# Kernel optimization log

Measured on AMD Instinct MI355X. Metric: run time of the kernel, lower is better.

## Reference

```python
import jax, jax.numpy as jnp
import numpy as np

B, L, D = 4, 256, 2048
LE, DE = 2048, 1024
H = 16
HD = D // H  # 128
ROPE_BASE = 10000.0


def apply_rope(q):
    # q: [B, H, L, HD]; rotate interleaved pairs along seq axis L (torchtune-style)
    half = HD // 2
    inv_freq = 1.0 / (ROPE_BASE ** (jnp.arange(0, HD, 2, dtype=jnp.float32) / HD))  # [half]
    pos = jnp.arange(L, dtype=jnp.float32)
    ang = pos[:, None] * inv_freq[None, :]           # [L, half]
    cos = jnp.cos(ang)[None, None, :, :]             # [1,1,L,half]
    sin = jnp.sin(ang)[None, None, :, :]
    qr = q.reshape(B, H, L, half, 2)
    q1, q2 = qr[..., 0], qr[..., 1]
    out = jnp.stack([q1 * cos - q2 * sin, q1 * sin + q2 * cos], axis=-1)
    return out.reshape(B, H, L, HD)


def setup_inputs() -> dict:
    key = jax.random.key(0)
    ks = jax.random.split(key, 7)
    s_d = 1.0 / np.sqrt(D)
    s_e = 1.0 / np.sqrt(DE)
    return {
        "x": jax.random.normal(ks[0], (B, L, D), jnp.float32),
        "encoder_inputs": jax.random.normal(ks[1], (B, LE, DE), jnp.float32),
        "Wq": jax.random.normal(ks[2], (D, D), jnp.float32) * s_d,
        "bq": jnp.zeros((D,), jnp.float32),
        "Wk": jax.random.normal(ks[3], (DE, D), jnp.float32) * s_e,
        "bk": jnp.zeros((D,), jnp.float32),
        "Wv": jax.random.normal(ks[4], (DE, D), jnp.float32) * s_e,
        "bv": jnp.zeros((D,), jnp.float32),
        "Wo": jax.random.normal(ks[5], (D, D), jnp.float32) * s_d,
        "bo": jnp.zeros((D,), jnp.float32),
    }


def reference(x, encoder_inputs, Wq, bq, Wk, bk, Wv, bv, Wo, bo):
    q = (x @ Wq + bq).reshape(B, L, H, HD).transpose(0, 2, 1, 3)              # [B,H,L,HD]
    k = (encoder_inputs @ Wk + bk).reshape(B, LE, H, HD).transpose(0, 2, 1, 3)  # [B,H,Le,HD]
    v = (encoder_inputs @ Wv + bv).reshape(B, LE, H, HD).transpose(0, 2, 1, 3)
    q = apply_rope(q)
    scale = 1.0 / jnp.sqrt(jnp.float32(HD))
    scores = jnp.einsum("bhld,bhmd->bhlm", q, k) * scale                      # [B,H,L,Le]
    attn = jax.nn.softmax(scores, axis=-1)
    ctx = jnp.einsum("bhlm,bhmd->bhld", attn, v)                              # [B,H,L,HD]
    ctx = ctx.transpose(0, 2, 1, 3).reshape(B, L, D)
    return ctx @ Wo + bo
```

## Files before the change

kernel.cpp:

```cpp
#include <hip/hip_runtime.h>


#define B_ 4
#define L_ 256
#define D_ 2048
#define LE_ 2048
#define DE_ 1024
#define H_ 16
#define HD_ 128

using f32x4  = __attribute__((ext_vector_type(4))) float;
using bf16x8 = __attribute__((ext_vector_type(8))) short;

__device__ __forceinline__ unsigned short f2bf(float f) {
    union { float f; unsigned int u; } v; v.f = f;
    unsigned int r = v.u + 0x7fffu + ((v.u >> 16) & 1u);
    return (unsigned short)(r >> 16);
}
__device__ __forceinline__ float b2f(unsigned short h) {
    union { unsigned int u; float f; } v; v.u = ((unsigned int)h) << 16;
    return v.f;
}

__device__ __forceinline__ void load_lds16(const void* g, void* l) {
    __builtin_amdgcn_global_load_lds((const __attribute__((address_space(1))) void*)g,
                                     (__attribute__((address_space(3))) void*)l, 16, 0, 0);
}

__global__ void cast_f32_bf16(const float* __restrict__ in, unsigned short* __restrict__ out, int n) {
    int i = (blockIdx.x * 256 + threadIdx.x) * 4;
    if (i < n) {
        float4 v = *(const float4*)(in + i);
        ushort4 o;
        o.x = f2bf(v.x); o.y = f2bf(v.y); o.z = f2bf(v.z); o.w = f2bf(v.w);
        *(ushort4*)(out + i) = o;
    }
}

__global__ void transpose_f32_bf16(const float* __restrict__ in, unsigned short* __restrict__ out,
                                   int R, int C) {
    __shared__ float t[32][33];
    int r0 = blockIdx.y * 32, c0 = blockIdx.x * 32;
    int tx = threadIdx.x, ty = threadIdx.y;
    #pragma unroll
    for (int i = 0; i < 32; i += 8) t[ty + i][tx] = in[(long)(r0 + ty + i) * C + c0 + tx];
    __syncthreads();
    #pragma unroll
    for (int i = 0; i < 32; i += 8) out[(long)(c0 + ty + i) * R + r0 + tx] = f2bf(t[tx][ty + i]);
}

__global__ void transpose_bf16_batched(const unsigned short* __restrict__ in,
                                       unsigned short* __restrict__ out, int R, int C) {
    __shared__ unsigned short t[32][33];
    long zo = (long)blockIdx.z * R * C;
    int r0 = blockIdx.y * 32, c0 = blockIdx.x * 32;
    int tx = threadIdx.x, ty = threadIdx.y;
    #pragma unroll
    for (int i = 0; i < 32; i += 8) t[ty + i][tx] = in[zo + (long)(r0 + ty + i) * C + c0 + tx];
    __syncthreads();
    #pragma unroll
    for (int i = 0; i < 32; i += 8) out[zo + (long)(c0 + ty + i) * R + r0 + tx] = t[tx][ty + i];
}

__global__ void combine_q_rope(const float* __restrict__ P, const float* __restrict__ bq,
                               unsigned short* __restrict__ Q) {
    int gid = blockIdx.x * 256 + threadIdx.x;
    int p = gid & 63;
    int h = (gid >> 6) & 15;
    int m = gid >> 10;
    int n = h * 128 + 2 * p;
    long i0 = (long)m * 2048 + n;
    float2 a  = *(const float2*)(P + i0);
    float2 b2 = *(const float2*)(P + 2097152 + i0);
    float q1 = a.x + b2.x + bq[n];
    float q2 = a.y + b2.y + bq[n + 1];
    int l = m & 255, b = m >> 8;
    float inv = powf(10000.0f, -(float)p * (1.0f / 64.0f));
    float s, c;
    sincosf((float)l * inv, &s, &c);
    const float sc = 0.08838834764831845f;
    long qi = (((long)(b * 16 + h) * 256 + l) << 7) + 2 * p;
    ushort2 o;
    o.x = f2bf((q1 * c - q2 * s) * sc);
    o.y = f2bf((q1 * s + q2 * c) * sc);
    *(ushort2*)(Q + qi) = o;
}

__global__ void combine_pv(const float* __restrict__ P, unsigned short* __restrict__ ctx) {
    int gid = blockIdx.x * 256 + threadIdx.x;
    long e = (long)gid * 4;
    float4 a = *(const float4*)(P + e);
    float4 b = *(const float4*)(P + 2097152 + e);
    int bh = (int)(e >> 15);
    int m  = (int)((e >> 7) & 255);
    int d  = (int)(e & 127);
    int bb = bh >> 4, h = bh & 15;
    ushort4 o;
    o.x = f2bf(a.x + b.x); o.y = f2bf(a.y + b.y);
    o.z = f2bf(a.z + b.z); o.w = f2bf(a.w + b.w);
    *(ushort4*)(ctx + ((long)(bb * 256 + m)) * 2048 + h * 128 + d) = o;
}

__global__ void combine_o(const float* __restrict__ P, const float* __restrict__ bo,
                          float* __restrict__ out) {
    int gid = blockIdx.x * 256 + threadIdx.x;
    long e = (long)gid * 4;
    float4 a = *(const float4*)(P + e);
    float4 b = *(const float4*)(P + 2097152 + e);
    int n = (int)(e & 2047);
    float4 bb = *(const float4*)(bo + n);
    float4 r;
    r.x = a.x + b.x + bb.x; r.y = a.y + b.y + bb.y;
    r.z = a.z + b.z + bb.z; r.w = a.w + b.w + bb.w;
    *(float4*)(out + e) = r;
}

__launch_bounds__(256)
__global__ void softmax_rows(unsigned short* __restrict__ S) {
    long row = blockIdx.x;
    unsigned short* p = S + row * 2048;
    int t = threadIdx.x, w = t >> 6, lane = t & 63;
    bf16x8 raw = *(const bf16x8*)(p + t * 8);
    float v[8];
    float mx = -1e30f;
    #pragma unroll
    for (int i = 0; i < 8; i++) { v[i] = b2f((unsigned short)raw[i]); mx = fmaxf(mx, v[i]); }
    #pragma unroll
    for (int o = 32; o; o >>= 1) mx = fmaxf(mx, __shfl_xor(mx, o));
    __shared__ float redm[4], reds[4];
    if (lane == 0) redm[w] = mx;
    __syncthreads();
    mx = fmaxf(fmaxf(redm[0], redm[1]), fmaxf(redm[2], redm[3]));
    float sum = 0.f;
    #pragma unroll
    for (int i = 0; i < 8; i++) { v[i] = __expf(v[i] - mx); sum += v[i]; }
    #pragma unroll
    for (int o = 32; o; o >>= 1) sum += __shfl_xor(sum, o);
    if (lane == 0) reds[w] = sum;
    __syncthreads();
    sum = reds[0] + reds[1] + reds[2] + reds[3];
    float r = 1.0f / sum;
    bf16x8 res;
    #pragma unroll
    for (int i = 0; i < 8; i++) res[i] = (short)f2bf(v[i] * r);
    *(bf16x8*)(p + t * 8) = res;
}

template <int EPI>
__launch_bounds__(256)
__global__ void gemm_bt(const unsigned short* __restrict__ A, const unsigned short* __restrict__ Bt,
                        const float* __restrict__ biasA, const float* __restrict__ biasB,
                        void* __restrict__ outA, void* __restrict__ outB,
                        int M, int N, int K, int lda, int ldb,
                        long strideA, long strideB, int zdiv, int nsplit) {
    __shared__ __align__(16) unsigned short smem[16384];
    const int z = blockIdx.z;
    int s = 0, bh = z;
    if constexpr (EPI == 4) { s = z / zdiv; bh = z - s * zdiv; }
    const unsigned short* Ab = A + (long)bh * strideA + (long)s * K;
    const unsigned short* Bb = Bt + (long)bh * strideB + (long)s * K;
    const int m0 = blockIdx.y * 128, n0 = blockIdx.x * 128;
    const int tid = threadIdx.x;
    const int w = tid >> 6, lane = tid & 63;
    const int quad = lane >> 4, l16 = lane & 15;
    const int wr = w >> 1, wc = w & 1;
    const int srow = lane >> 2;
    const int scol = (lane & 3) * 8;

    f32x4 acc[4][4] = {};

    auto stage = [&](int k0, int p) {
        unsigned short* As = smem + p * 8192;
        unsigned short* Bs = As + 4096;
        #pragma unroll
        for (int q = 0; q < 2; q++) {
            int ci = q * 4 + w;
            int row = ci * 16 + srow;
            load_lds16(Ab + (long)(m0 + row) * lda + k0 + scol, (void*)(As + ci * 512));
            load_lds16(Bb + (long)(n0 + row) * ldb + k0 + scol, (void*)(Bs + ci * 512));
        }
    };

    const int nk = K >> 5;
    stage(0, 0);
    for (int i = 0; i < nk; i++) {
        __syncthreads();
        if (i + 1 < nk) stage((i + 1) << 5, (i + 1) & 1);
        const unsigned short* As = smem + (i & 1) * 8192;
        const unsigned short* Bs = As + 4096;
        bf16x8 af[4], bfr[4];
        #pragma unroll
        for (int ii = 0; ii < 4; ii++) {
            int r = wr * 64 + ii * 16 + l16;
            af[ii] = *(const bf16x8*)(As + r * 32 + quad * 8);
        }
        #pragma unroll
        for (int j = 0; j < 4; j++) {
            int r = wc * 64 + j * 16 + l16;
            bfr[j] = *(const bf16x8*)(Bs + r * 32 + quad * 8);
        }
        #pragma unroll
        for (int ii = 0; ii < 4; ii++)
            #pragma unroll
            for (int j = 0; j < 4; j++)
                acc[ii][j] = __builtin_amdgcn_mfma_f32_16x16x32_bf16(af[ii], bfr[j], acc[ii][j], 0, 0, 0);
    }
    __syncthreads();

    if constexpr (EPI == 1 || EPI == 2) {
        const bool second = (EPI == 1) && (n0 >= nsplit);
        const float* bias = second ? biasB : biasA;
        const int n0e = second ? n0 - nsplit : n0;
        unsigned short* dst = (unsigned short*)(second ? outB : outA);
        #pragma unroll
        for (int p = 0; p < 2; p++) {
            if (wr == p) {
                #pragma unroll
                for (int i = 0; i < 4; i++)
                    #pragma unroll
                    for (int j = 0; j < 4; j++)
                        #pragma unroll
                        for (int r = 0; r < 4; r++) {
                            int ml = i * 16 + quad * 4 + r;
                            int n  = wc * 64 + j * 16 + l16;
                            float v = acc[i][j][r];
                            if (bias) v += bias[n0e + n];
                            smem[ml * 136 + n] = f2bf(v);
                        }
            }
            __syncthreads();
            #pragma unroll
            for (int pass = 0; pass < 4; pass++) {
                int row = pass * 16 + (tid >> 4);
                int seg = tid & 15;
                bf16x8 val = *(const bf16x8*)(smem + row * 136 + seg * 8);
                int m = m0 + p * 64 + row;
                if constexpr (EPI == 1) {
                    int h = n0e >> 7;
                    int b = m >> 11, mrow = m & 2047;
                    long idx = (((long)(b * 16 + h)) << 11) + mrow;
                    *(bf16x8*)(dst + (idx << 7) + seg * 8) = val;
                } else {
                    *(bf16x8*)((unsigned short*)outA + (long)z * M * N + (long)m * N + n0 + seg * 8) = val;
                }
            }
            __syncthreads();
        }
    } else {
        float* smf = (float*)smem;
        long zo = ((long)s * zdiv + bh) * (long)M * N;
        #pragma unroll
        for (int q4 = 0; q4 < 4; q4++) {
            if (wr == (q4 >> 1)) {
                #pragma unroll
                for (int ii = 0; ii < 2; ii++) {
                    int i = (q4 & 1) * 2 + ii;
                    #pragma unroll
                    for (int j = 0; j < 4; j++)
                        #pragma unroll
                        for (int r = 0; r < 4; r++) {
                            int ml = ii * 16 + quad * 4 + r;
                            int n  = wc * 64 + j * 16 + l16;
                            smf[ml * 132 + n] = acc[i][j][r];
                        }
                }
            }
            __syncthreads();
            #pragma unroll
            for (int pass = 0; pass < 4; pass++) {
                int row = pass * 8 + (tid >> 5);
                int seg = tid & 31;
                float4 val = *(const float4*)(smf + row * 132 + seg * 4);
                int m = m0 + q4 * 32 + row;
                *(float4*)((float*)outA + zo + (long)m * N + n0 + seg * 4) = val;
            }
            __syncthreads();
        }
    }
}

extern "C" void kernel_launch(void* const* d_in, const int* in_sizes, int n_in,
                              void* d_out, int out_size, void* d_ws, size_t ws_size,
                              hipStream_t stream) {
    const float* x   = (const float*)d_in[0];
    const float* enc = (const float*)d_in[1];
    const float* Wq  = (const float*)d_in[2];
    const float* bq  = (const float*)d_in[3];
    const float* Wk  = (const float*)d_in[4];
    const float* bk  = (const float*)d_in[5];
    const float* Wv  = (const float*)d_in[6];
    const float* bv  = (const float*)d_in[7];
    const float* Wo  = (const float*)d_in[8];
    const float* bo  = (const float*)d_in[9];
    float* out = (float*)d_out;

    char* ws = (char*)d_ws;
    const size_t MB = 1024 * 1024;
    unsigned short* x_bf   = (unsigned short*)(ws + 0 * MB);
    unsigned short* enc_bf = (unsigned short*)(ws + 4 * MB);
    unsigned short* WqT    = (unsigned short*)(ws + 20 * MB);
    unsigned short* WkvT   = (unsigned short*)(ws + 28 * MB);
    unsigned short* V_bf   = (unsigned short*)(ws + 36 * MB);
    unsigned short* K_bf   = (unsigned short*)(ws + 68 * MB);
    unsigned short* WoT    = (unsigned short*)(ws + 100 * MB);
    unsigned short* Q_bf   = (unsigned short*)(ws + 108 * MB);
    unsigned short* Vt     = (unsigned short*)(ws + 112 * MB);
    unsigned short* S_bf   = (unsigned short*)(ws + 0 * MB);
    float*          Pq     = (float*)(ws + 36 * MB);
    float*          Ppv    = (float*)(ws + 68 * MB);
    float*          Po     = (float*)(ws + 0 * MB);
    unsigned short* ctx_bf = (unsigned short*)(ws + 108 * MB);

    dim3 tb(32, 8);

    cast_f32_bf16<<<2048, 256, 0, stream>>>(x, x_bf, 2097152);
    cast_f32_bf16<<<8192, 256, 0, stream>>>(enc, enc_bf, 8388608);

    transpose_f32_bf16<<<dim3(64, 64), tb, 0, stream>>>(Wq, WqT, 2048, 2048);
    transpose_f32_bf16<<<dim3(64, 32), tb, 0, stream>>>(Wk, WkvT, 1024, 2048);
    transpose_f32_bf16<<<dim3(64, 32), tb, 0, stream>>>(Wv, WkvT + 2048 * 1024, 1024, 2048);
    transpose_f32_bf16<<<dim3(64, 64), tb, 0, stream>>>(Wo, WoT, 2048, 2048);

    gemm_bt<4><<<dim3(16, 8, 2), 256, 0, stream>>>(x_bf, WqT, nullptr, nullptr, Pq, nullptr,
                                                   1024, 2048, 1024, 2048, 2048, 0, 0, 1, 0);
    combine_q_rope<<<4096, 256, 0, stream>>>(Pq, bq, Q_bf);

    gemm_bt<1><<<dim3(32, 64, 1), 256, 0, stream>>>(enc_bf, WkvT, bk, bv, K_bf, V_bf,
                                                    8192, 4096, 1024, 1024, 1024, 0, 0, 1, 2048);

    transpose_bf16_batched<<<dim3(4, 64, 64), tb, 0, stream>>>(V_bf, Vt, 2048, 128);

    gemm_bt<2><<<dim3(16, 2, 64), 256, 0, stream>>>(Q_bf, K_bf, nullptr, nullptr, S_bf, nullptr,
                                                    256, 2048, 128, 128, 128,
                                                    256 * 128, 2048 * 128, 1, 0);
    softmax_rows<<<16384, 256, 0, stream>>>(S_bf);

    gemm_bt<4><<<dim3(1, 2, 128), 256, 0, stream>>>(S_bf, Vt, nullptr, nullptr, Ppv, nullptr,
                                                    256, 128, 1024, 2048, 2048,
                                                    256 * 2048, 128 * 2048, 64, 0);
    combine_pv<<<2048, 256, 0, stream>>>(Ppv, ctx_bf);

    gemm_bt<4><<<dim3(16, 8, 2), 256, 0, stream>>>(ctx_bf, WoT, nullptr, nullptr, Po, nullptr,
                                                   1024, 2048, 1024, 2048, 2048, 0, 0, 1, 0);
    combine_o<<<2048, 256, 0, stream>>>(Po, bo, out);
}
```

Before: 404.2 us.

## Load GEMM fragments directly from global into registers, dropping LDS staging

The GEMM main loop no longer stages A/B tiles through LDS with global_load_lds. Each wave now loads its MFMA fragments straight from global memory into registers, using a two-deep register double buffer, and the per-iteration barriers are removed. LDS usage drops, which may raise occupancy. In exchange there is no data sharing across waves, so each A/B row is fetched by two waves and global and L2 traffic increases.

```diff
diff --git a/kernel.cpp b/kernel.cpp
--- a/kernel.cpp
+++ b/kernel.cpp
@@ -20,11 +20,6 @@
 __device__ __forceinline__ float b2f(unsigned short h) {
     union { unsigned int u; float f; } v; v.u = ((unsigned int)h) << 16;
     return v.f;
-}
-
-__device__ __forceinline__ void load_lds16(const void* g, void* l) {
-    __builtin_amdgcn_global_load_lds((const __attribute__((address_space(1))) void*)g,
-                                     (__attribute__((address_space(3))) void*)l, 16, 0, 0);
 }
 
 __global__ void cast_f32_bf16(const float* __restrict__ in, unsigned short* __restrict__ out, int n) {
@@ -153,7 +148,7 @@
                         void* __restrict__ outA, void* __restrict__ outB,
                         int M, int N, int K, int lda, int ldb,
                         long strideA, long strideB, int zdiv, int nsplit) {
-    __shared__ __align__(16) unsigned short smem[16384];
+    __shared__ __align__(16) unsigned short smem[8704];
     const int z = blockIdx.z;
     int s = 0, bh = z;
     if constexpr (EPI == 4) { s = z / zdiv; bh = z - s * zdiv; }
@@ -164,48 +159,46 @@
     const int w = tid >> 6, lane = tid & 63;
     const int quad = lane >> 4, l16 = lane & 15;
     const int wr = w >> 1, wc = w & 1;
-    const int srow = lane >> 2;
-    const int scol = (lane & 3) * 8;
+
+    const unsigned short* Arow[4];
+    const unsigned short* Brow[4];
+    #pragma unroll
+    for (int i = 0; i < 4; i++)
+        Arow[i] = Ab + (long)(m0 + wr * 64 + i * 16 + l16) * lda + quad * 8;
+    #pragma unroll
+    for (int j = 0; j < 4; j++)
+        Brow[j] = Bb + (long)(n0 + wc * 64 + j * 16 + l16) * ldb + quad * 8;
 
     f32x4 acc[4][4] = {};
-
-    auto stage = [&](int k0, int p) {
-        unsigned short* As = smem + p * 8192;
-        unsigned short* Bs = As + 4096;
-        #pragma unroll
-        for (int q = 0; q < 2; q++) {
-            int ci = q * 4 + w;
-            int row = ci * 16 + srow;
-            load_lds16(Ab + (long)(m0 + row) * lda + k0 + scol, (void*)(As + ci * 512));
-            load_lds16(Bb + (long)(n0 + row) * ldb + k0 + scol, (void*)(Bs + ci * 512));
+    bf16x8 a0[4], b0[4], a1[4], b1[4];
+
+    #pragma unroll
+    for (int i = 0; i < 4; i++) a0[i] = *(const bf16x8*)(Arow[i]);
+    #pragma unroll
+    for (int j = 0; j < 4; j++) b0[j] = *(const bf16x8*)(Brow[j]);
+
+    for (int k = 0; k + 64 <= K; k += 64) {
+        #pragma unroll
+        for (int i = 0; i < 4; i++) a1[i] = *(const bf16x8*)(Arow[i] + k + 32);
+        #pragma unroll
+        for (int j = 0; j < 4; j++) b1[j] = *(const bf16x8*)(Brow[j] + k + 32);
+        #pragma unroll
+        for (int i = 0; i < 4; i++)
+            #pragma unroll
+            for (int j = 0; j < 4; j++)
+                acc[i][j] = __builtin_amdgcn_mfma_f32_16x16x32_bf16(a0[i], b0[j], acc[i][j], 0, 0, 0);
+        if (k + 64 < K) {
+            #pragma unroll
+            for (int i = 0; i < 4; i++) a0[i] = *(const bf16x8*)(Arow[i] + k + 64);
+            #pragma unroll
+            for (int j = 0; j < 4; j++) b0[j] = *(const bf16x8*)(Brow[j] + k + 64);
         }
-    };
-
-    const int nk = K >> 5;
-    stage(0, 0);
-    for (int i = 0; i < nk; i++) {
-        __syncthreads();
-        if (i + 1 < nk) stage((i + 1) << 5, (i + 1) & 1);
-        const unsigned short* As = smem + (i & 1) * 8192;
-        const unsigned short* Bs = As + 4096;
-        bf16x8 af[4], bfr[4];
-        #pragma unroll
-        for (int ii = 0; ii < 4; ii++) {
-            int r = wr * 64 + ii * 16 + l16;
-            af[ii] = *(const bf16x8*)(As + r * 32 + quad * 8);
-        }
-        #pragma unroll
-        for (int j = 0; j < 4; j++) {
-            int r = wc * 64 + j * 16 + l16;
-            bfr[j] = *(const bf16x8*)(Bs + r * 32 + quad * 8);
-        }
-        #pragma unroll
-        for (int ii = 0; ii < 4; ii++)
+        #pragma unroll
+        for (int i = 0; i < 4; i++)
             #pragma unroll
             for (int j = 0; j < 4; j++)
-                acc[ii][j] = __builtin_amdgcn_mfma_f32_16x16x32_bf16(af[ii], bfr[j], acc[ii][j], 0, 0, 0);
+                acc[i][j] = __builtin_amdgcn_mfma_f32_16x16x32_bf16(a1[i], b1[j], acc[i][j], 0, 0, 0);
     }
-    __syncthreads();
 
     if constexpr (EPI == 1 || EPI == 2) {
         const bool second = (EPI == 1) && (n0 >= nsplit);
```

Result: slower. 609.3 us (+50.8%).

## Triple-buffer GEMM LDS pipeline with vmcnt waits and raise split-K to four

Applied to the files above, without the earlier changes.

The GEMM main loop moves from double to triple buffering in shared memory. It prefetches two K-tiles ahead and uses explicit s_waitcnt vmcnt plus a raw barrier instead of a full __syncthreads, so global-to-LDS loads overlap more with MFMA work. The Q, PV and O projections also go from two to four split-K partitions to launch more blocks, and the combine kernels now sum four partials. The cost is more LDS per block (48KB), which can lower occupancy, and twice the partial-sum traffic through global memory in the combine kernels.

```diff
diff --git a/kernel.cpp b/kernel.cpp
--- a/kernel.cpp
+++ b/kernel.cpp
@@ -70,10 +70,12 @@
     int m = gid >> 10;
     int n = h * 128 + 2 * p;
     long i0 = (long)m * 2048 + n;
-    float2 a  = *(const float2*)(P + i0);
-    float2 b2 = *(const float2*)(P + 2097152 + i0);
-    float q1 = a.x + b2.x + bq[n];
-    float q2 = a.y + b2.y + bq[n + 1];
+    float q1 = bq[n], q2 = bq[n + 1];
+    #pragma unroll
+    for (int pt = 0; pt < 4; pt++) {
+        float2 a = *(const float2*)(P + (long)pt * 2097152 + i0);
+        q1 += a.x; q2 += a.y;
+    }
     int l = m & 255, b = m >> 8;
     float inv = powf(10000.0f, -(float)p * (1.0f / 64.0f));
     float s, c;
@@ -90,14 +92,17 @@
     int gid = blockIdx.x * 256 + threadIdx.x;
     long e = (long)gid * 4;
     float4 a = *(const float4*)(P + e);
-    float4 b = *(const float4*)(P + 2097152 + e);
+    #pragma unroll
+    for (int pt = 1; pt < 4; pt++) {
+        float4 b = *(const float4*)(P + (long)pt * 2097152 + e);
+        a.x += b.x; a.y += b.y; a.z += b.z; a.w += b.w;
+    }
     int bh = (int)(e >> 15);
     int m  = (int)((e >> 7) & 255);
     int d  = (int)(e & 127);
     int bb = bh >> 4, h = bh & 15;
     ushort4 o;
-    o.x = f2bf(a.x + b.x); o.y = f2bf(a.y + b.y);
-    o.z = f2bf(a.z + b.z); o.w = f2bf(a.w + b.w);
+    o.x = f2bf(a.x); o.y = f2bf(a.y); o.z = f2bf(a.z); o.w = f2bf(a.w);
     *(ushort4*)(ctx + ((long)(bb * 256 + m)) * 2048 + h * 128 + d) = o;
 }
 
@@ -105,13 +110,13 @@
                           float* __restrict__ out) {
     int gid = blockIdx.x * 256 + threadIdx.x;
     long e = (long)gid * 4;
-    float4 a = *(const float4*)(P + e);
-    float4 b = *(const float4*)(P + 2097152 + e);
     int n = (int)(e & 2047);
-    float4 bb = *(const float4*)(bo + n);
-    float4 r;
-    r.x = a.x + b.x + bb.x; r.y = a.y + b.y + bb.y;
-    r.z = a.z + b.z + bb.z; r.w = a.w + b.w + bb.w;
+    float4 r = *(const float4*)(bo + n);
+    #pragma unroll
+    for (int pt = 0; pt < 4; pt++) {
+        float4 a = *(const float4*)(P + (long)pt * 2097152 + e);
+        r.x += a.x; r.y += a.y; r.z += a.z; r.w += a.w;
+    }
     *(float4*)(out + e) = r;
 }
 
@@ -153,7 +158,7 @@
                         void* __restrict__ outA, void* __restrict__ outB,
                         int M, int N, int K, int lda, int ldb,
                         long strideA, long strideB, int zdiv, int nsplit) {
-    __shared__ __align__(16) unsigned short smem[16384];
+    __shared__ __align__(16) unsigned short smem[24576];
     const int z = blockIdx.z;
     int s = 0, bh = z;
     if constexpr (EPI == 4) { s = z / zdiv; bh = z - s * zdiv; }
@@ -183,10 +188,17 @@
 
     const int nk = K >> 5;
     stage(0, 0);
+    stage(32, 1);
+    int p = 0;
     for (int i = 0; i < nk; i++) {
-        __syncthreads();
-        if (i + 1 < nk) stage((i + 1) << 5, (i + 1) & 1);
-        const unsigned short* As = smem + (i & 1) * 8192;
+        if (i + 1 < nk) asm volatile("s_waitcnt vmcnt(4)" ::: "memory");
+        else            asm volatile("s_waitcnt vmcnt(0)" ::: "memory");
+        __builtin_amdgcn_s_barrier();
+        if (i + 2 < nk) {
+            int pn = p + 2; if (pn >= 3) pn -= 3;
+            stage((i + 2) << 5, pn);
+        }
+        const unsigned short* As = smem + p * 8192;
         const unsigned short* Bs = As + 4096;
         bf16x8 af[4], bfr[4];
         #pragma unroll
@@ -204,6 +216,7 @@
             #pragma unroll
             for (int j = 0; j < 4; j++)
                 acc[ii][j] = __builtin_amdgcn_mfma_f32_16x16x32_bf16(af[ii], bfr[j], acc[ii][j], 0, 0, 0);
+        if (++p >= 3) p -= 3;
     }
     __syncthreads();
 
@@ -213,8 +226,8 @@
         const int n0e = second ? n0 - nsplit : n0;
         unsigned short* dst = (unsigned short*)(second ? outB : outA);
         #pragma unroll
-        for (int p = 0; p < 2; p++) {
-            if (wr == p) {
+        for (int pp = 0; pp < 2; pp++) {
+            if (wr == pp) {
                 #pragma unroll
                 for (int i = 0; i < 4; i++)
                     #pragma unroll
@@ -234,7 +247,7 @@
                 int row = pass * 16 + (tid >> 4);
                 int seg = tid & 15;
                 bf16x8 val = *(const bf16x8*)(smem + row * 136 + seg * 8);
-                int m = m0 + p * 64 + row;
+                int m = m0 + pp * 64 + row;
                 if constexpr (EPI == 1) {
                     int h = n0e >> 7;
                     int b = m >> 11, mrow = m & 2047;
@@ -321,8 +334,8 @@
     transpose_f32_bf16<<<dim3(64, 32), tb, 0, stream>>>(Wv, WkvT + 2048 * 1024, 1024, 2048);
     transpose_f32_bf16<<<dim3(64, 64), tb, 0, stream>>>(Wo, WoT, 2048, 2048);
 
-    gemm_bt<4><<<dim3(16, 8, 2), 256, 0, stream>>>(x_bf, WqT, nullptr, nullptr, Pq, nullptr,
-                                                   1024, 2048, 1024, 2048, 2048, 0, 0, 1, 0);
+    gemm_bt<4><<<dim3(16, 8, 4), 256, 0, stream>>>(x_bf, WqT, nullptr, nullptr, Pq, nullptr,
+                                                   1024, 2048, 512, 2048, 2048, 0, 0, 1, 0);
     combine_q_rope<<<4096, 256, 0, stream>>>(Pq, bq, Q_bf);
 
     gemm_bt<1><<<dim3(32, 64, 1), 256, 0, stream>>>(enc_bf, WkvT, bk, bv, K_bf, V_bf,
@@ -335,12 +348,12 @@
                                                     256 * 128, 2048 * 128, 1, 0);
     softmax_rows<<<16384, 256, 0, stream>>>(S_bf);
 
-    gemm_bt<4><<<dim3(1, 2, 128), 256, 0, stream>>>(S_bf, Vt, nullptr, nullptr, Ppv, nullptr,
-                                                    256, 128, 1024, 2048, 2048,
+    gemm_bt<4><<<dim3(1, 2, 256), 256, 0, stream>>>(S_bf, Vt, nullptr, nullptr, Ppv, nullptr,
+                                                    256, 128, 512, 2048, 2048,
                                                     256 * 2048, 128 * 2048, 64, 0);
     combine_pv<<<2048, 256, 0, stream>>>(Ppv, ctx_bf);
 
-    gemm_bt<4><<<dim3(16, 8, 2), 256, 0, stream>>>(ctx_bf, WoT, nullptr, nullptr, Po, nullptr,
-                                                   1024, 2048, 1024, 2048, 2048, 0, 0, 1, 0);
+    gemm_bt<4><<<dim3(16, 8, 4), 256, 0, stream>>>(ctx_bf, WoT, nullptr, nullptr, Po, nullptr,
+                                                   1024, 2048, 512, 2048, 2048, 0, 0, 1, 0);
     combine_o<<<2048, 256, 0, stream>>>(Po, bo, out);
 }
```

Result: no change. 406.0 us (+0.5%).
